# Performance work log

Hardware: AMD Instinct MI355X
Metric: run time of the kernel (lower is better)

Reference implementation:

```python
import jax, jax.numpy as jnp
import numpy as np

B, CIN, G, H, HW, WMIX = 128, 64, 8, 14, 16, 16  # batch, in-ch, groups, spatial, mixed width


def setup_inputs() -> dict:
    key = jax.random.key(0)
    k1, k2, k3 = jax.random.split(key, 3)
    x = jax.random.normal(k1, (B, CIN, G, H, H), dtype=jnp.float32)
    w_conv = jax.random.normal(k2, (G, 3, 3, 32), dtype=jnp.float32)   # weights[0]
    w_mix = jax.random.normal(k3, (CIN, WMIX), dtype=jnp.float32)       # weights[1]
    return {"x": x, "w_conv": w_conv, "w_mix": w_mix}


def _unfold3(t, axis, size):
    # torch F.unfold with kernel (3,1), padding (1,0) along `axis`: zero-pad by 1
    # and stack the 3 shifted windows as a new axis inserted at `axis`.
    pad = [(0, 0)] * t.ndim
    pad[axis] = (1, 1)
    p = jnp.pad(t, pad)
    slices = []
    for k in range(3):
        idx = [slice(None)] * t.ndim
        idx[axis] = slice(k, k + size)
        slices.append(p[tuple(idx)])
    return jnp.stack(slices, axis=axis)


def reference(x, w_conv, w_mix):
    # channel mix: (B, 64, 8, 14, 14) x (64, 16) -> (B, 8, 14, 14, 16)
    t4 = jnp.einsum('kjmnl,ji->kmnli', x, w_mix)
    # first unfold along H (axis 3): (B, 8, 14, 3, 14, 16)
    u1 = _unfold3(t4, 3, H)
    # second unfold along H (now axis 4): (B, 8, 14, 3, 3, 14, 16)
    u2 = _unfold3(u1, 4, H)
    # permute (0,1,2,5,4,3,6) -> (B, 8, 14, 14, 3, 3, 16)
    t5 = jnp.transpose(u2, (0, 1, 2, 5, 4, 3, 6))
    # conv channel mix: contract group(8) and both 3-taps -> (B, 14, 14, 16, 32)
    t6 = jnp.einsum('mlonikp,likj->monpj', t5, w_conv)
    # (B, 14, 14, 32, 16) -> (B, 14, 14, 512)
    t7 = jnp.transpose(t6, (0, 1, 2, 4, 3)).reshape(B, H, H, 512)
    t7 = jnp.roll(t7, 1, axis=1)  # shift_direction fixed to +1
    return jnp.transpose(t7, (0, 3, 1, 2))  # (B, 512, 14, 14)
```

## Files before the change

### kernel.cpp

```cpp
#include <hip/hip_runtime.h>

static constexpr int NB   = 128;
static constexpr int NCIN = 64;
static constexpr int NG   = 8;
static constexpr int NH   = 14;
static constexpr int NP   = 16;
static constexpr int HH   = NH * NH;
static constexpr int LROW = 20;

static constexpr int OFF_W2 = 0;
static constexpr int OFF_WC = 1280;
static constexpr int OFF_T4 = 1792;
static constexpr int OFF_XS = 4352;
static constexpr int OFF_WM = 8384;
static constexpr int LDS_FLOATS = 9408;

__global__ __launch_bounds__(256) void fused_kernel(const float* __restrict__ x,
                                                    const float* __restrict__ wconv,
                                                    const float* __restrict__ wmix,
                                                    float* __restrict__ out) {
    __shared__ __align__(16) float lds[LDS_FLOATS];
    float*  w2s = lds + OFF_W2;
    float*  wcs = lds + OFF_WC;
    float*  t4s = lds + OFF_T4;
    float4* xs4 = reinterpret_cast<float4*>(lds + OFF_XS);
    float4* wm4 = reinterpret_cast<float4*>(lds + OFF_WM);

    const int tid   = threadIdx.x;
    const int b     = blockIdx.x / NH;
    const int o     = blockIdx.x % NH;
    const int o_src = (o + NH - 1) % NH;

    const float* xb = x + (size_t)b * (NCIN * NG * HH) + o_src * NH;

    float xr[14];
#pragma unroll
    for (int r = 0; r < 14; r++) {
        int idx = r * 256 + tid;
        int j   = idx / 112;
        int gl  = idx % 112;
        xr[r] = xb[(size_t)j * (NG * HH) + (gl / 14) * HH + (gl % 14)];
    }

#pragma unroll
    for (int r = 0; r < 4; r++) {
        int idx = r * 256 + tid;
        int jw  = idx >> 6;
        int p   = (idx >> 2) & 15;
        int jj  = idx & 3;
        lds[OFF_WM + idx] = wmix[(jw * 4 + jj) * NP + p];
    }
#pragma unroll
    for (int r = 0; r < 5; r++) {
        int idx = r * 256 + tid;
        int g   = idx / 160;
        int di  = (idx / 32) % 5;
        int j   = idx % 32;
        int ilo = di > 2 ? di - 2 : 0;
        int ihi = di < 2 ? di : 2;
        float s = 0.f;
        for (int i = ilo; i <= ihi; i++) {
            int k = di - i;
            s += wconv[((g * 3 + i) * 3 + k) * 32 + j];
        }
        w2s[idx] = s;
    }
#pragma unroll
    for (int r = 0; r < 2; r++) {
        int idx = r * 256 + tid;
        int sel = idx / 256;
        int g   = (idx / 32) % 8;
        int j   = idx % 32;
        wcs[idx] = wconv[(g * 9 + (sel ? 6 : 2)) * 32 + j];
    }
#pragma unroll
    for (int r = 0; r < 3; r++) {
        int idx = r * 256 + tid;
        int gp  = idx / 6;
        int s   = idx % 6;
        int l2  = (s < 2) ? s : (14 + s);
        t4s[gp * LROW + l2] = 0.f;
    }
#pragma unroll
    for (int r = 0; r < 14; r++) {
        int idx  = r * 256 + tid;
        int j    = idx / 112;
        int gl   = idx % 112;
        int glst = gl + (gl >> 3);
        lds[OFF_XS + (((j >> 2) * 126 + glst) << 2) + (j & 3)] = xr[r];
    }
    __syncthreads();

#pragma unroll
    for (int r = 0; r < 14; r++) {
        int idx = r * 256 + tid;
        int j   = 32 + idx / 112;
        int gl  = idx % 112;
        xr[r] = xb[(size_t)j * (NG * HH) + (gl / 14) * HH + (gl % 14)];
    }

    const int  glp   = tid >> 2;
    const int  pq    = tid & 3;
    const bool bact  = (glp < 56);
    const int  glst0 = glp + (glp >> 3);
    const int  glst1 = glst0 + 63;
    float accA[4] = {0.f, 0.f, 0.f, 0.f};
    float accB[4] = {0.f, 0.f, 0.f, 0.f};

    if (bact) {
#pragma unroll
        for (int j4 = 0; j4 < 8; j4++) {
            float4 xa = xs4[j4 * 126 + glst0];
            float4 xv = xs4[j4 * 126 + glst1];
#pragma unroll
            for (int pp = 0; pp < 4; pp++) {
                float4 w = wm4[j4 * 16 + pq * 4 + pp];
                accA[pp] += xa.x * w.x + xa.y * w.y + xa.z * w.z + xa.w * w.w;
                accB[pp] += xv.x * w.x + xv.y * w.y + xv.z * w.z + xv.w * w.w;
            }
        }
    }
    __syncthreads();
#pragma unroll
    for (int r = 0; r < 14; r++) {
        int idx  = r * 256 + tid;
        int j    = idx / 112;
        int gl   = idx % 112;
        int glst = gl + (gl >> 3);
        lds[OFF_XS + (((j >> 2) * 126 + glst) << 2) + (j & 3)] = xr[r];
    }
    __syncthreads();

    if (bact) {
#pragma unroll
        for (int j4 = 0; j4 < 8; j4++) {
            float4 xa = xs4[j4 * 126 + glst0];
            float4 xv = xs4[j4 * 126 + glst1];
#pragma unroll
            for (int pp = 0; pp < 4; pp++) {
                float4 w = wm4[(8 + j4) * 16 + pq * 4 + pp];
                accA[pp] += xa.x * w.x + xa.y * w.y + xa.z * w.z + xa.w * w.w;
                accB[pp] += xv.x * w.x + xv.y * w.y + xv.z * w.z + xv.w * w.w;
            }
        }
        int g0 = glp / 14,        l0 = glp % 14;
        int g1 = (glp + 56) / 14, l1 = (glp + 56) % 14;
#pragma unroll
        for (int pp = 0; pp < 4; pp++) {
            t4s[(g0 * 16 + pq * 4 + pp) * LROW + l0 + 2] = accA[pp];
            t4s[(g1 * 16 + pq * 4 + pp) * LROW + l1 + 2] = accB[pp];
        }
    }
    __syncthreads();

    const int p  = tid & 15;
    const int jh = tid >> 4;
    const int jb = jh * 2;

    float acc[NH][2];
#pragma unroll
    for (int n = 0; n < NH; n++) { acc[n][0] = 0.f; acc[n][1] = 0.f; }

    for (int g = 0; g < NG; g++) {
        float row[LROW];
        const float* rp = &t4s[(g * 16 + p) * LROW];
#pragma unroll
        for (int q = 0; q < 5; q++) {
            float4 v = *reinterpret_cast<const float4*>(rp + q * 4);
            row[q * 4 + 0] = v.x; row[q * 4 + 1] = v.y;
            row[q * 4 + 2] = v.z; row[q * 4 + 3] = v.w;
        }
#pragma unroll
        for (int di = 0; di < 5; di++) {
            float2 w = *reinterpret_cast<const float2*>(&w2s[(g * 5 + di) * 32 + jb]);
#pragma unroll
            for (int n = 0; n < NH; n++) {
                float rv = row[n + di];
                acc[n][0] += rv * w.x;
                acc[n][1] += rv * w.y;
            }
        }
        float2 c0 = *reinterpret_cast<const float2*>(&wcs[g * 32 + jb]);
        float2 c1 = *reinterpret_cast<const float2*>(&wcs[256 + g * 32 + jb]);
        float r2 = row[2], r15 = row[15];
        acc[0][0]  -= r2  * c0.x; acc[0][1]  -= r2  * c0.y;
        acc[13][0] -= r15 * c1.x; acc[13][1] -= r15 * c1.y;
    }

    __syncthreads();

#pragma unroll
    for (int jj = 0; jj < 2; jj++) {
        int cl  = (jb + jj) * 16 + p;
        int rot = (cl >> 5) * 2;
        int sb  = cl * 15;
#pragma unroll
        for (int n = 0; n < NH; n++) {
            int rn = n + rot;
            rn -= (rn >= 15) ? 15 : 0;
            rn -= (rn >= 15) ? 15 : 0;
            lds[sb + rn] = acc[n][jj];
        }
    }
    __syncthreads();

    float* ob = out + (size_t)b * 512 * HH + (size_t)o * NH;
#pragma unroll
    for (int r = 0; r < 28; r++) {
        int idx = r * 256 + tid;
        int c   = idx / 14;
        int n   = idx % 14;
        int rn  = n + (c >> 5) * 2;
        rn -= (rn >= 15) ? 15 : 0;
        rn -= (rn >= 15) ? 15 : 0;
        ob[(size_t)c * HH + n] = lds[c * 15 + rn];
    }
}

extern "C" void kernel_launch(void* const* d_in, const int* in_sizes, int n_in,
                              void* d_out, int out_size, void* d_ws, size_t ws_size,
                              hipStream_t stream) {
    const float* x     = (const float*)d_in[0];
    const float* wconv = (const float*)d_in[1];
    const float* wmix  = (const float*)d_in[2];
    float* out = (float*)d_out;
    (void)d_ws; (void)ws_size;

    fused_kernel<<<NB * NH, 256, 0, stream>>>(x, wconv, wmix, out);
}
```

Measured before the change: 147.2 us.

## Read wmix as wave-uniform scalar loads instead of staging it in LDS

Removes the LDS staging of the channel-mix weights. The mix stage is remapped so each wave handles 64 spatial positions and a wave-uniform block of 8 output channels, with p0 made uniform via readfirstlane. The weight reads become uniform global loads that the compiler can turn into scalar (SMEM) loads, which drops the per-thread LDS weight reads and shrinks the LDS footprint. The cost is many more scalar loads and some idle lanes (112 of 128 positions are active per wave pair), in exchange for fewer LDS reads and possibly higher occupancy.

```diff
diff --git a/kernel.cpp b/kernel.cpp
--- a/kernel.cpp
+++ b/kernel.cpp
@@ -12,8 +12,7 @@
 static constexpr int OFF_WC = 1280;
 static constexpr int OFF_T4 = 1792;
 static constexpr int OFF_XS = 4352;
-static constexpr int OFF_WM = 8384;
-static constexpr int LDS_FLOATS = 9408;
+static constexpr int LDS_FLOATS = 8384;
 
 __global__ __launch_bounds__(256) void fused_kernel(const float* __restrict__ x,
                                                     const float* __restrict__ wconv,
@@ -24,7 +23,6 @@
     float*  wcs = lds + OFF_WC;
     float*  t4s = lds + OFF_T4;
     float4* xs4 = reinterpret_cast<float4*>(lds + OFF_XS);
-    float4* wm4 = reinterpret_cast<float4*>(lds + OFF_WM);
 
     const int tid   = threadIdx.x;
     const int b     = blockIdx.x / NH;
@@ -42,14 +40,6 @@
         xr[r] = xb[(size_t)j * (NG * HH) + (gl / 14) * HH + (gl % 14)];
     }
 
-#pragma unroll
-    for (int r = 0; r < 4; r++) {
-        int idx = r * 256 + tid;
-        int jw  = idx >> 6;
-        int p   = (idx >> 2) & 15;
-        int jj  = idx & 3;
-        lds[OFF_WM + idx] = wmix[(jw * 4 + jj) * NP + p];
-    }
 #pragma unroll
     for (int r = 0; r < 5; r++) {
         int idx = r * 256 + tid;
@@ -99,24 +89,25 @@
         xr[r] = xb[(size_t)j * (NG * HH) + (gl / 14) * HH + (gl % 14)];
     }
 
-    const int  glp   = tid >> 2;
-    const int  pq    = tid & 3;
-    const bool bact  = (glp < 56);
-    const int  glst0 = glp + (glp >> 3);
-    const int  glst1 = glst0 + 63;
-    float accA[4] = {0.f, 0.f, 0.f, 0.f};
-    float accB[4] = {0.f, 0.f, 0.f, 0.f};
+    const int  wv   = tid >> 6;
+    const int  glB  = ((wv & 1) << 6) + (tid & 63);
+    const bool bact = (glB < 112);
+    const int  p0   = __builtin_amdgcn_readfirstlane((tid >> 7) << 3);
+    const int  glst = glB + (glB >> 3);
+
+    float am[8] = {0.f, 0.f, 0.f, 0.f, 0.f, 0.f, 0.f, 0.f};
 
     if (bact) {
 #pragma unroll
         for (int j4 = 0; j4 < 8; j4++) {
-            float4 xa = xs4[j4 * 126 + glst0];
-            float4 xv = xs4[j4 * 126 + glst1];
-#pragma unroll
-            for (int pp = 0; pp < 4; pp++) {
-                float4 w = wm4[j4 * 16 + pq * 4 + pp];
-                accA[pp] += xa.x * w.x + xa.y * w.y + xa.z * w.z + xa.w * w.w;
-                accB[pp] += xv.x * w.x + xv.y * w.y + xv.z * w.z + xv.w * w.w;
+            float4 xq = xs4[j4 * 126 + glst];
+#pragma unroll
+            for (int pp = 0; pp < 8; pp++) {
+                const int p = p0 + pp;
+                am[pp] += xq.x * wmix[(j4 * 4 + 0) * NP + p]
+                        + xq.y * wmix[(j4 * 4 + 1) * NP + p]
+                        + xq.z * wmix[(j4 * 4 + 2) * NP + p]
+                        + xq.w * wmix[(j4 * 4 + 3) * NP + p];
             }
         }
     }
@@ -126,29 +117,29 @@
         int idx  = r * 256 + tid;
         int j    = idx / 112;
         int gl   = idx % 112;
-        int glst = gl + (gl >> 3);
-        lds[OFF_XS + (((j >> 2) * 126 + glst) << 2) + (j & 3)] = xr[r];
+        int glst2 = gl + (gl >> 3);
+        lds[OFF_XS + (((j >> 2) * 126 + glst2) << 2) + (j & 3)] = xr[r];
     }
     __syncthreads();
 
     if (bact) {
+        const float* wm1 = wmix + 32 * NP;
 #pragma unroll
         for (int j4 = 0; j4 < 8; j4++) {
-            float4 xa = xs4[j4 * 126 + glst0];
-            float4 xv = xs4[j4 * 126 + glst1];
-#pragma unroll
-            for (int pp = 0; pp < 4; pp++) {
-                float4 w = wm4[(8 + j4) * 16 + pq * 4 + pp];
-                accA[pp] += xa.x * w.x + xa.y * w.y + xa.z * w.z + xa.w * w.w;
-                accB[pp] += xv.x * w.x + xv.y * w.y + xv.z * w.z + xv.w * w.w;
+            float4 xq = xs4[j4 * 126 + glst];
+#pragma unroll
+            for (int pp = 0; pp < 8; pp++) {
+                const int p = p0 + pp;
+                am[pp] += xq.x * wm1[(j4 * 4 + 0) * NP + p]
+                        + xq.y * wm1[(j4 * 4 + 1) * NP + p]
+                        + xq.z * wm1[(j4 * 4 + 2) * NP + p]
+                        + xq.w * wm1[(j4 * 4 + 3) * NP + p];
             }
         }
-        int g0 = glp / 14,        l0 = glp % 14;
-        int g1 = (glp + 56) / 14, l1 = (glp + 56) % 14;
-#pragma unroll
-        for (int pp = 0; pp < 4; pp++) {
-            t4s[(g0 * 16 + pq * 4 + pp) * LROW + l0 + 2] = accA[pp];
-            t4s[(g1 * 16 + pq * 4 + pp) * LROW + l1 + 2] = accB[pp];
+        int g = glB / 14, l = glB % 14;
+#pragma unroll
+        for (int pp = 0; pp < 8; pp++) {
+            t4s[(g * 16 + p0 + pp) * LROW + l + 2] = am[pp];
         }
     }
     __syncthreads();
```

New measurement: 140.8 us. 4.4% less time.
